# Kernel optimization log

Hardware: AMD Instinct MI355X
Metric: run time of the kernel (lower is better)

Reference implementation:

```python
import jax, jax.numpy as jnp
import numpy as np

E, M, B, S = 1024, 256, 4, 2048
LN_EPS = 1e-5

def _l2norm(x):
    # F.normalize(p=2, dim=-1, eps=1e-12)
    n = jnp.linalg.norm(x, axis=-1, keepdims=True)
    return x / jnp.maximum(n, 1e-12)

def _layernorm(x, g, b):
    mu = jnp.mean(x, axis=-1, keepdims=True)
    var = jnp.var(x, axis=-1, keepdims=True)
    return (x - mu) * jax.lax.rsqrt(var + LN_EPS) * g + b

def setup_inputs() -> dict:
    key = jax.random.key(0)
    ks = jax.random.split(key, 16)
    s = 0.02
    inp = {
        'x': jax.random.normal(ks[0], (B, S, E), jnp.float32),
        'memory': jnp.zeros((B, M, M), jnp.float32),
        'w_k': jax.random.normal(ks[1], (M, E), jnp.float32) * s,
        'b_k': jnp.zeros((M,), jnp.float32),
        'w_q': jax.random.normal(ks[2], (M, E), jnp.float32) * s,
        'b_q': jnp.zeros((M,), jnp.float32),
        'w_v': jax.random.normal(ks[3], (M, E), jnp.float32) * s,
        'b_v': jnp.zeros((M,), jnp.float32),
        'w_out': jax.random.normal(ks[4], (E, M), jnp.float32) * s,
        'b_out': jnp.zeros((E,), jnp.float32),
        'w_gw': jax.random.normal(ks[5], (1, E), jnp.float32) * s,
        'b_gw': jnp.full((1,), -2.0, jnp.float32),
        'w_gf': jax.random.normal(ks[6], (1, E), jnp.float32) * s,
        'b_gf': jnp.full((1,), 2.0, jnp.float32),
        'ln1_g': jnp.ones((E,), jnp.float32),
        'ln1_b': jnp.zeros((E,), jnp.float32),
        'ln2_g': jnp.ones((E,), jnp.float32),
        'ln2_b': jnp.zeros((E,), jnp.float32),
        'w_f1': jax.random.normal(ks[7], (4 * E, E), jnp.float32) * s,
        'b_f1': jnp.zeros((4 * E,), jnp.float32),
        'w_f2': jax.random.normal(ks[8], (E, 4 * E), jnp.float32) * s,
        'b_f2': jnp.zeros((E,), jnp.float32),
    }
    return inp

def reference(x, memory, w_k, b_k, w_q, b_q, w_v, b_v, w_out, b_out,
              w_gw, b_gw, w_gf, b_gf, ln1_g, ln1_b, ln2_g, ln2_b,
              w_f1, b_f1, w_f2, b_f2):
    xn = _layernorm(x, ln1_g, ln1_b)                      # [B,S,E]
    k_all = _l2norm(xn @ w_k.T + b_k)                     # [B,S,M]
    q_all = _l2norm(xn @ w_q.T + b_q)                     # [B,S,M]
    v_all = jnp.tanh(xn @ w_v.T + b_v)                    # [B,S,M]
    beta_all = jax.nn.sigmoid(xn @ w_gw.T + b_gw)         # [B,S,1]
    decay_all = jax.nn.sigmoid(xn @ w_gf.T + b_gf)        # [B,S,1]

    def step(mem, inps):
        k, q, v, beta, decay = inps                       # k,q,v:[B,M]; beta,decay:[B,1]
        readout = jnp.einsum('bij,bj->bi', mem, q)        # read BEFORE update
        assoc = v[:, :, None] * k[:, None, :]             # [B,M,M] outer product
        mem = decay[:, :, None] * mem + beta[:, :, None] * assoc
        return mem, readout

    seq = (jnp.swapaxes(k_all, 0, 1), jnp.swapaxes(q_all, 0, 1),
           jnp.swapaxes(v_all, 0, 1), jnp.swapaxes(beta_all, 0, 1),
           jnp.swapaxes(decay_all, 0, 1))
    new_memory, readouts = jax.lax.scan(step, memory, seq)  # readouts: [S,B,M]
    stacked = jnp.swapaxes(readouts, 0, 1)                  # [B,S,M]
    mixer_out = stacked @ w_out.T + b_out                   # [B,S,E]

    x = x + mixer_out
    h = _layernorm(x, ln2_g, ln2_b)
    ffn = jax.nn.gelu(h @ w_f1.T + b_f1, approximate=False) @ w_f2.T + b_f2
    x = x + ffn
    return (x, new_memory)
```

## Files before the change

### kernel.cpp

```cpp
#include <hip/hip_runtime.h>
#include <stdint.h>

#define E_DIM 1024
#define M_DIM 256
#define B_DIM 4
#define S_DIM 2048
#define NTOK  8192
#define CHUNK 64
#define NCHUNK 32
#define NCB   128

typedef unsigned short u16;
typedef unsigned int   u32;
typedef __attribute__((ext_vector_type(8))) short short8;
typedef __attribute__((ext_vector_type(4))) float floatx4;

#define OFF_WKQV   ((size_t)0)
#define OFF_WOUT   ((size_t)1572864)
#define OFF_WF1    ((size_t)2097152)
#define OFF_WF2    ((size_t)10485760)
#define OFF_BKQV   ((size_t)18874368)
#define OFF_BETA   ((size_t)18877440)
#define OFF_DECAY  ((size_t)18910208)
#define OFF_P      ((size_t)18942976)
#define OFF_WW     ((size_t)18976256)
#define OFF_ABUF   ((size_t)19009024)
#define OFF_XN     ((size_t)21106176)
#define OFF_KQV    ((size_t)37883392)
#define OFF_T      ((size_t)63049216)
#define OFF_STATES ((size_t)96603648)
#define OFF_RO     ((size_t)130158080)
#define OFF_H      OFF_XN
#define OFF_Y1     OFF_T
#define OFF_G      OFF_STATES

__device__ __forceinline__ u16 f2bf(float f) {
    union { float f; u32 u; } a; a.f = f;
    u32 u = a.u;
    return (u16)((u + 0x7fffu + ((u >> 16) & 1u)) >> 16);
}
__device__ __forceinline__ u32 pack2bf(float a, float b) {
    return (u32)f2bf(a) | ((u32)f2bf(b) << 16);
}
__device__ __forceinline__ float sigmoidf_(float x) { return 1.0f / (1.0f + expf(-x)); }

__device__ __forceinline__ void gload_lds16(const u16* g, u16* l) {
    __builtin_amdgcn_global_load_lds((const __attribute__((address_space(1))) void*)g,
                                     (__attribute__((address_space(3))) void*)l, 16, 0, 0);
}

__device__ __forceinline__ void block_reduce_2(float& a, float& b, float* red, int t) {
#pragma unroll
    for (int o = 32; o > 0; o >>= 1) { a += __shfl_xor(a, o); b += __shfl_xor(b, o); }
    if ((t & 63) == 0) { red[t >> 6] = a; red[4 + (t >> 6)] = b; }
    __syncthreads();
    a = red[0] + red[1] + red[2] + red[3];
    b = red[4] + red[5] + red[6] + red[7];
    __syncthreads();
}

__global__ void f2bf4_kernel(const float4* __restrict__ in, uint2* __restrict__ out, int n4) {
    int i = blockIdx.x * 256 + threadIdx.x;
    if (i < n4) {
        float4 v = in[i];
        uint2 o; o.x = pack2bf(v.x, v.y); o.y = pack2bf(v.z, v.w);
        out[i] = o;
    }
}
__global__ void pack_kqv_w(const float4* __restrict__ wk, const float4* __restrict__ wq,
                           const float4* __restrict__ wv, uint2* __restrict__ out) {
    int i = blockIdx.x * 256 + threadIdx.x;
    int sec = i >> 16;
    int off = i & 65535;
    const float4* src = (sec == 0) ? wk : ((sec == 1) ? wq : wv);
    float4 v = src[off];
    uint2 o; o.x = pack2bf(v.x, v.y); o.y = pack2bf(v.z, v.w);
    out[i] = o;
}
__global__ void pack_bias(const float* __restrict__ bk, const float* __restrict__ bq,
                          const float* __restrict__ bv, float* __restrict__ out) {
    int i = blockIdx.x * 256 + threadIdx.x;
    if (i < 256) out[i] = bk[i];
    else if (i < 512) out[i] = bq[i - 256];
    else out[i] = bv[i - 512];
}

__global__ __launch_bounds__(256) void ln1_gates(
    const float* __restrict__ x, const float* __restrict__ g, const float* __restrict__ b,
    const float* __restrict__ wgw, const float* __restrict__ bgw,
    const float* __restrict__ wgf, const float* __restrict__ bgf,
    u16* __restrict__ xn, float* __restrict__ beta, float* __restrict__ decay)
{
    __shared__ float red[8];
    const int row = blockIdx.x;
    const int t = threadIdx.x;
    const float4 v = ((const float4*)(x + (size_t)row * E_DIM))[t];
    float s  = v.x + v.y + v.z + v.w;
    float ss = v.x * v.x + v.y * v.y + v.z * v.z + v.w * v.w;
    block_reduce_2(s, ss, red, t);
    const float mean = s * (1.0f / E_DIM);
    const float var  = ss * (1.0f / E_DIM) - mean * mean;
    const float rstd = rsqrtf(var + 1e-5f);
    const float4 gg = ((const float4*)g)[t];
    const float4 bb = ((const float4*)b)[t];
    float4 xnv;
    xnv.x = (v.x - mean) * rstd * gg.x + bb.x;
    xnv.y = (v.y - mean) * rstd * gg.y + bb.y;
    xnv.z = (v.z - mean) * rstd * gg.z + bb.z;
    xnv.w = (v.w - mean) * rstd * gg.w + bb.w;
    uint2 o; o.x = pack2bf(xnv.x, xnv.y); o.y = pack2bf(xnv.z, xnv.w);
    ((uint2*)(xn + (size_t)row * E_DIM))[t] = o;
    const float4 w1 = ((const float4*)wgw)[t];
    const float4 w2 = ((const float4*)wgf)[t];
    float dg = xnv.x * w1.x + xnv.y * w1.y + xnv.z * w1.z + xnv.w * w1.w;
    float df = xnv.x * w2.x + xnv.y * w2.y + xnv.z * w2.z + xnv.w * w2.w;
    block_reduce_2(dg, df, red, t);
    if (t == 0) {
        beta[row]  = sigmoidf_(dg + bgw[0]);
        decay[row] = sigmoidf_(df + bgf[0]);
    }
}

__global__ __launch_bounds__(256) void ln2_kernel(
    const float* __restrict__ y1, const float* __restrict__ g, const float* __restrict__ b,
    u16* __restrict__ h)
{
    __shared__ float red[8];
    const int row = blockIdx.x;
    const int t = threadIdx.x;
    const float4 v = ((const float4*)(y1 + (size_t)row * E_DIM))[t];
    float s  = v.x + v.y + v.z + v.w;
    float ss = v.x * v.x + v.y * v.y + v.z * v.z + v.w * v.w;
    block_reduce_2(s, ss, red, t);
    const float mean = s * (1.0f / E_DIM);
    const float var  = ss * (1.0f / E_DIM) - mean * mean;
    const float rstd = rsqrtf(var + 1e-5f);
    const float4 gg = ((const float4*)g)[t];
    const float4 bb = ((const float4*)b)[t];
    float4 xnv;
    xnv.x = (v.x - mean) * rstd * gg.x + bb.x;
    xnv.y = (v.y - mean) * rstd * gg.y + bb.y;
    xnv.z = (v.z - mean) * rstd * gg.z + bb.z;
    xnv.w = (v.w - mean) * rstd * gg.w + bb.w;
    uint2 o; o.x = pack2bf(xnv.x, xnv.y); o.y = pack2bf(xnv.z, xnv.w);
    ((uint2*)(h + (size_t)row * E_DIM))[t] = o;
}

__global__ __launch_bounds__(256) void kqv_act(float* __restrict__ kqv) {
    __shared__ float red[8];
    const int row = blockIdx.x;
    const int t = threadIdx.x;
    float* p = kqv + (size_t)row * 768;
    float kv = p[t], qv = p[256 + t], vv = p[512 + t];
    float sk = kv * kv, sq = qv * qv;
    block_reduce_2(sk, sq, red, t);
    float nk = fmaxf(sqrtf(sk), 1e-12f);
    float nq = fmaxf(sqrtf(sq), 1e-12f);
    p[t]       = kv / nk;
    p[256 + t] = qv / nq;
    p[512 + t] = tanhf(vv);
}

__global__ void chunk_prep(const float* __restrict__ beta, const float* __restrict__ decay,
                           float* __restrict__ P, float* __restrict__ ww) {
    int cb = blockIdx.x;
    int b = cb >> 5, c = cb & 31;
    int tb = b * S_DIM + c * CHUNK;
    int j = threadIdx.x;
    __shared__ float d[64], bt[64], Ps[65];
    d[j]  = decay[tb + j];
    bt[j] = beta[tb + j];
    __syncthreads();
    if (j == 0) {
        float p = 1.0f; Ps[0] = 1.0f;
        for (int i = 0; i < 64; i++) { p *= d[i]; Ps[i + 1] = p; }
    }
    __syncthreads();
    P[cb * 65 + j] = Ps[j];
    if (j == 0) P[cb * 65 + 64] = Ps[64];
    ww[cb * 64 + j] = bt[j] / Ps[j + 1];
}

__global__ __launch_bounds__(256) void t_kernel(const float* __restrict__ kqv,
                                                const float* __restrict__ P,
                                                const float* __restrict__ ww,
                                                float* __restrict__ T) {
    int cb = blockIdx.y;
    int tile = blockIdx.x;
    int r0 = (tile >> 2) * 64, c0 = (tile & 3) * 64;
    int b = cb >> 5, c = cb & 31;
    int tb = b * S_DIM + c * CHUNK;
    float p64 = P[cb * 65 + 64];
    __shared__ float Vs[64][65], Ks[64][65];
    int t = threadIdx.x;
#pragma unroll
    for (int i = 0; i < 16; i++) {
        int idx = t + i * 256; int j = idx >> 6, col = idx & 63;
        float sc = ww[cb * 64 + j] * p64;
        Vs[j][col] = kqv[(size_t)(tb + j) * 768 + 512 + r0 + col] * sc;
        Ks[j][col] = kqv[(size_t)(tb + j) * 768 + 0   + c0 + col];
    }
    __syncthreads();
    int tr = t >> 4, tc = t & 15;
    float a[4][4] = {};
    for (int j = 0; j < 64; j++) {
        float vv[4], kk[4];
#pragma unroll
        for (int r = 0; r < 4; r++)  vv[r] = Vs[j][tr * 4 + r];
#pragma unroll
        for (int cc = 0; cc < 4; cc++) kk[cc] = Ks[j][tc * 4 + cc];
#pragma unroll
        for (int r = 0; r < 4; r++)
#pragma unroll
            for (int cc = 0; cc < 4; cc++) a[r][cc] += vv[r] * kk[cc];
    }
#pragma unroll
    for (int r = 0; r < 4; r++)
#pragma unroll
        for (int cc = 0; cc < 4; cc++)
            T[(size_t)cb * 65536 + (size_t)(r0 + tr * 4 + r) * 256 + (c0 + tc * 4 + cc)] = a[r][cc];
}

__global__ void mem_scan(const float* __restrict__ mem0, const float* __restrict__ T,
                         const float* __restrict__ P, float* __restrict__ states,
                         float* __restrict__ memOut) {
    int gid = blockIdx.x * 256 + threadIdx.x;
    int b = gid >> 16; int e = gid & 65535;
    float s = mem0[gid];
    for (int c = 0; c < NCHUNK; c++) {
        int cb = b * NCHUNK + c;
        states[(size_t)cb * 65536 + e] = s;
        s = P[cb * 65 + 64] * s + T[(size_t)cb * 65536 + e];
    }
    memOut[gid] = s;
}

__global__ __launch_bounds__(256) void qk_attn(const float* __restrict__ kqv,
                                               const float* __restrict__ P,
                                               const float* __restrict__ ww,
                                               float* __restrict__ Abuf) {
    int cb = blockIdx.x;
    int b = cb >> 5, c = cb & 31;
    int tb = b * S_DIM + c * CHUNK;
    __shared__ float Qs[64][65], Ks[64][65];
    int t = threadIdx.x;
    int tr = t >> 4, tc = t & 15;
    float acc[4][4] = {};
    for (int kt = 0; kt < 4; kt++) {
        __syncthreads();
#pragma unroll
        for (int i = 0; i < 16; i++) {
            int idx = t + i * 256; int rr = idx >> 6, cc2 = idx & 63;
            Qs[rr][cc2] = kqv[(size_t)(tb + rr) * 768 + 256 + kt * 64 + cc2];
            Ks[rr][cc2] = kqv[(size_t)(tb + rr) * 768 + 0   + kt * 64 + cc2];
        }
        __syncthreads();
        for (int kk = 0; kk < 64; kk++) {
            float qq[4], kx[4];
#pragma unroll
            for (int r = 0; r < 4; r++)  qq[r] = Qs[tr * 4 + r][kk];
#pragma unroll
            for (int cc = 0; cc < 4; cc++) kx[cc] = Ks[tc * 4 + cc][kk];
#pragma unroll
            for (int r = 0; r < 4; r++)
#pragma unroll
                for (int cc = 0; cc < 4; cc++) acc[r][cc] += qq[r] * kx[cc];
        }
    }
#pragma unroll
    for (int r = 0; r < 4; r++) {
#pragma unroll
        for (int cc = 0; cc < 4; cc++) {
            int i = tr * 4 + r, j = tc * 4 + cc;
            float v = (j < i) ? acc[r][cc] * (P[cb * 65 + i] * ww[cb * 64 + j]) : 0.0f;
            Abuf[(size_t)cb * 4096 + i * 64 + j] = v;
        }
    }
}

__global__ __launch_bounds__(256) void readout_k(const float* __restrict__ kqv,
                                                 const float* __restrict__ Abuf,
                                                 const float* __restrict__ states,
                                                 const float* __restrict__ P,
                                                 u16* __restrict__ ro) {
    int cb = blockIdx.y;
    int rt = blockIdx.x;
    int b = cb >> 5, c = cb & 31;
    int tb = b * S_DIM + c * CHUNK;
    int r0 = rt * 64;
    __shared__ float As[64][65], Vs[64][65], Qs[64][65], Ms[64][65];
    int t = threadIdx.x;
    int tr = t >> 4, tc = t & 15;
#pragma unroll
    for (int i = 0; i < 16; i++) {
        int idx = t + i * 256; int rr = idx >> 6, cc2 = idx & 63;
        As[rr][cc2] = Abuf[(size_t)cb * 4096 + rr * 64 + cc2];
        Vs[rr][cc2] = kqv[(size_t)(tb + rr) * 768 + 512 + r0 + cc2];
    }
    __syncthreads();
    float acc[4][4] = {};
    for (int j = 0; j < 64; j++) {
        float aa[4], vv[4];
#pragma unroll
        for (int r = 0; r < 4; r++)  aa[r] = As[tr * 4 + r][j];
#pragma unroll
        for (int cc = 0; cc < 4; cc++) vv[cc] = Vs[j][tc * 4 + cc];
#pragma unroll
        for (int r = 0; r < 4; r++)
#pragma unroll
            for (int cc = 0; cc < 4; cc++) acc[r][cc] += aa[r] * vv[cc];
    }
    float acc2[4][4] = {};
    for (int kt = 0; kt < 4; kt++) {
        __syncthreads();
#pragma unroll
        for (int i = 0; i < 16; i++) {
            int idx = t + i * 256; int rr = idx >> 6, cc2 = idx & 63;
            Qs[rr][cc2] = kqv[(size_t)(tb + rr) * 768 + 256 + kt * 64 + cc2];
            Ms[rr][cc2] = states[(size_t)cb * 65536 + (size_t)(r0 + rr) * 256 + kt * 64 + cc2];
        }
        __syncthreads();
        for (int kk = 0; kk < 64; kk++) {
            float qq[4], mm[4];
#pragma unroll
            for (int r = 0; r < 4; r++)  qq[r] = Qs[tr * 4 + r][kk];
#pragma unroll
            for (int cc = 0; cc < 4; cc++) mm[cc] = Ms[tc * 4 + cc][kk];
#pragma unroll
            for (int r = 0; r < 4; r++)
#pragma unroll
                for (int cc = 0; cc < 4; cc++) acc2[r][cc] += qq[r] * mm[cc];
        }
    }
#pragma unroll
    for (int r = 0; r < 4; r++) {
#pragma unroll
        for (int cc = 0; cc < 4; cc++) {
            int i = tr * 4 + r;
            float val = acc[r][cc] + P[cb * 65 + i] * acc2[r][cc];
            ro[(size_t)(tb + i) * 256 + r0 + tc * 4 + cc] = f2bf(val);
        }
    }
}

#define EPI_BIAS  0
#define EPI_RESID 1
#define EPI_GELU  2

template<int EPI>
__global__ __launch_bounds__(256) void gemm_bt(
    const u16* __restrict__ A, int lda,
    const u16* __restrict__ B, int ldb,
    const float* __restrict__ bias,
    const float* __restrict__ resid,
    float* __restrict__ outF, u16* __restrict__ outB,
    int ldc, int K)
{
    __shared__ u16 As[2][64 * 32];
    __shared__ u16 Bs[2][128 * 32];
    const int t = threadIdx.x;
    const int lane = t & 63;
    const int w = t >> 6;
    const int waveM = (w >> 1) * 32;
    const int waveN = (w & 1) * 64;
    const int m0 = blockIdx.y * 64;
    const int n0 = blockIdx.x * 128;

    const int sr = t >> 2, sc = (t & 3) * 8;
    const u16* Ag  = A + (size_t)(m0 + sr) * lda + sc;
    const u16* Bg0 = B + (size_t)(n0 + sr) * ldb + sc;
    const u16* Bg1 = B + (size_t)(n0 + 64 + sr) * ldb + sc;

    floatx4 acc[2][4] = {};

    const int kg = (lane >> 4) * 8;
    const int rsel = lane & 15;
    const int NK = K >> 5;

    gload_lds16(Ag, As[0] + t * 8);
    gload_lds16(Bg0, Bs[0] + t * 8);
    gload_lds16(Bg1, Bs[0] + (t + 256) * 8);

    for (int kt = 0; kt < NK; kt++) {
        __syncthreads();
        const int cur = kt & 1;
        if (kt + 1 < NK) {
            const int kof = (kt + 1) * 32;
            gload_lds16(Ag + kof, As[cur ^ 1] + t * 8);
            gload_lds16(Bg0 + kof, Bs[cur ^ 1] + t * 8);
            gload_lds16(Bg1 + kof, Bs[cur ^ 1] + (t + 256) * 8);
        }
        short8 af[2], bfr[4];
#pragma unroll
        for (int i = 0; i < 2; i++)
            af[i] = *(const short8*)(As[cur] + (waveM + i * 16 + rsel) * 32 + kg);
#pragma unroll
        for (int j = 0; j < 4; j++)
            bfr[j] = *(const short8*)(Bs[cur] + (waveN + j * 16 + rsel) * 32 + kg);
#pragma unroll
        for (int i = 0; i < 2; i++)
#pragma unroll
            for (int j = 0; j < 4; j++)
                acc[i][j] = __builtin_amdgcn_mfma_f32_16x16x32_bf16(af[i], bfr[j], acc[i][j], 0, 0, 0);
    }

    const int rbase = (lane >> 4) * 4;
#pragma unroll
    for (int i = 0; i < 2; i++) {
#pragma unroll
        for (int j = 0; j < 4; j++) {
            const int col = n0 + waveN + j * 16 + rsel;
            const float bv = bias[col];
#pragma unroll
            for (int r = 0; r < 4; r++) {
                const int row = m0 + waveM + i * 16 + rbase + r;
                const size_t oidx = (size_t)row * ldc + col;
                float v = acc[i][j][r] + bv;
                if (EPI == EPI_BIAS) {
                    outF[oidx] = v;
                } else if (EPI == EPI_RESID) {
                    outF[oidx] = v + resid[oidx];
                } else {
                    float gl = 0.5f * v * (1.0f + erff(v * 0.70710678118654752f));
                    outB[oidx] = f2bf(gl);
                }
            }
        }
    }
}

extern "C" void kernel_launch(void* const* d_in, const int* in_sizes, int n_in,
                              void* d_out, int out_size, void* d_ws, size_t ws_size,
                              hipStream_t stream) {
    const float* x     = (const float*)d_in[0];
    const float* mem0  = (const float*)d_in[1];
    const float* w_k   = (const float*)d_in[2];
    const float* b_k   = (const float*)d_in[3];
    const float* w_q   = (const float*)d_in[4];
    const float* b_q   = (const float*)d_in[5];
    const float* w_v   = (const float*)d_in[6];
    const float* b_v   = (const float*)d_in[7];
    const float* w_out = (const float*)d_in[8];
    const float* b_out = (const float*)d_in[9];
    const float* w_gw  = (const float*)d_in[10];
    const float* b_gw  = (const float*)d_in[11];
    const float* w_gf  = (const float*)d_in[12];
    const float* b_gf  = (const float*)d_in[13];
    const float* ln1g  = (const float*)d_in[14];
    const float* ln1b  = (const float*)d_in[15];
    const float* ln2g  = (const float*)d_in[16];
    const float* ln2b  = (const float*)d_in[17];
    const float* w_f1  = (const float*)d_in[18];
    const float* b_f1  = (const float*)d_in[19];
    const float* w_f2  = (const float*)d_in[20];
    const float* b_f2  = (const float*)d_in[21];

    char* ws = (char*)d_ws;
    u16*   wkqv  = (u16*)(ws + OFF_WKQV);
    u16*   wout  = (u16*)(ws + OFF_WOUT);
    u16*   wf1   = (u16*)(ws + OFF_WF1);
    u16*   wf2   = (u16*)(ws + OFF_WF2);
    float* bkqv  = (float*)(ws + OFF_BKQV);
    float* beta  = (float*)(ws + OFF_BETA);
    float* decay = (float*)(ws + OFF_DECAY);
    float* P     = (float*)(ws + OFF_P);
    float* ww    = (float*)(ws + OFF_WW);
    float* Abuf  = (float*)(ws + OFF_ABUF);
    u16*   xn    = (u16*)(ws + OFF_XN);
    float* kqv   = (float*)(ws + OFF_KQV);
    float* T     = (float*)(ws + OFF_T);
    float* states= (float*)(ws + OFF_STATES);
    u16*   ro    = (u16*)(ws + OFF_RO);
    u16*   h     = (u16*)(ws + OFF_H);
    float* y1    = (float*)(ws + OFF_Y1);
    u16*   g     = (u16*)(ws + OFF_G);

    float* out_x   = (float*)d_out;
    float* out_mem = out_x + (size_t)NTOK * E_DIM;

    pack_kqv_w<<<768, 256, 0, stream>>>((const float4*)w_k, (const float4*)w_q,
                                        (const float4*)w_v, (uint2*)wkqv);
    f2bf4_kernel<<<256, 256, 0, stream>>>((const float4*)w_out, (uint2*)wout, 1024 * 256 / 4);
    f2bf4_kernel<<<4096, 256, 0, stream>>>((const float4*)w_f1, (uint2*)wf1, 4096 * 1024 / 4);
    f2bf4_kernel<<<4096, 256, 0, stream>>>((const float4*)w_f2, (uint2*)wf2, 1024 * 4096 / 4);
    pack_bias<<<3, 256, 0, stream>>>(b_k, b_q, b_v, bkqv);

    ln1_gates<<<NTOK, 256, 0, stream>>>(x, ln1g, ln1b, w_gw, b_gw, w_gf, b_gf, xn, beta, decay);

    gemm_bt<EPI_BIAS><<<dim3(6, 128), 256, 0, stream>>>(xn, 1024, wkqv, 1024, bkqv, nullptr,
                                                        kqv, nullptr, 768, 1024);
    kqv_act<<<NTOK, 256, 0, stream>>>(kqv);

    chunk_prep<<<NCB, 64, 0, stream>>>(beta, decay, P, ww);
    t_kernel<<<dim3(16, NCB), 256, 0, stream>>>(kqv, P, ww, T);
    mem_scan<<<1024, 256, 0, stream>>>(mem0, T, P, states, out_mem);
    qk_attn<<<NCB, 256, 0, stream>>>(kqv, P, ww, Abuf);
    readout_k<<<dim3(4, NCB), 256, 0, stream>>>(kqv, Abuf, states, P, ro);

    gemm_bt<EPI_RESID><<<dim3(8, 128), 256, 0, stream>>>(ro, 256, wout, 256, b_out, x,
                                                         y1, nullptr, 1024, 256);
    ln2_kernel<<<NTOK, 256, 0, stream>>>(y1, ln2g, ln2b, h);
    gemm_bt<EPI_GELU><<<dim3(32, 128), 256, 0, stream>>>(h, 1024, wf1, 1024, b_f1, nullptr,
                                                         nullptr, g, 4096, 1024);
    gemm_bt<EPI_RESID><<<dim3(8, 128), 256, 0, stream>>>(g, 4096, wf2, 4096, b_f2, y1,
                                                         out_x, nullptr, 1024, 4096);
}
```

Measured before the change: 539.3 us.

## Swizzle GEMM LDS layout and use 128-row tiles for FFN1 GEMM

```diff
diff --git a/kernel.cpp b/kernel.cpp
--- a/kernel.cpp
+++ b/kernel.cpp
@@ -47,6 +47,13 @@
 __device__ __forceinline__ void gload_lds16(const u16* g, u16* l) {
     __builtin_amdgcn_global_load_lds((const __attribute__((address_space(1))) void*)g,
                                      (__attribute__((address_space(3))) void*)l, 16, 0, 0);
+}
+
+__device__ __forceinline__ int sw_slot(int idx) {
+    return ((idx & 3) ^ ((idx >> 3) & 3)) * 8;
+}
+__device__ __forceinline__ int sw_read(int row, int kc) {
+    return row * 32 + ((kc ^ ((row >> 1) & 3)) << 3);
 }
 
 __device__ __forceinline__ void block_reduce_2(float& a, float& b, float* red, int t) {
@@ -347,7 +354,7 @@
 #define EPI_RESID 1
 #define EPI_GELU  2
 
-template<int EPI>
+template<int EPI, int BM>
 __global__ __launch_bounds__(256) void gemm_bt(
     const u16* __restrict__ A, int lda,
     const u16* __restrict__ B, int ldb,
@@ -356,28 +363,31 @@
     float* __restrict__ outF, u16* __restrict__ outB,
     int ldc, int K)
 {
-    __shared__ u16 As[2][64 * 32];
+    constexpr int MI = BM / 32;
+    __shared__ u16 As[2][BM * 32];
     __shared__ u16 Bs[2][128 * 32];
     const int t = threadIdx.x;
     const int lane = t & 63;
     const int w = t >> 6;
-    const int waveM = (w >> 1) * 32;
+    const int waveM = (w >> 1) * (BM / 2);
     const int waveN = (w & 1) * 64;
-    const int m0 = blockIdx.y * 64;
+    const int m0 = blockIdx.y * BM;
     const int n0 = blockIdx.x * 128;
 
-    const int sr = t >> 2, sc = (t & 3) * 8;
-    const u16* Ag  = A + (size_t)(m0 + sr) * lda + sc;
-    const u16* Bg0 = B + (size_t)(n0 + sr) * ldb + sc;
-    const u16* Bg1 = B + (size_t)(n0 + 64 + sr) * ldb + sc;
-
-    floatx4 acc[2][4] = {};
-
-    const int kg = (lane >> 4) * 8;
+    const int sr = t >> 2, scw = sw_slot(t);
+    const u16* Ag0 = A + (size_t)(m0 + sr) * lda + scw;
+    const u16* Ag1 = A + (size_t)(m0 + 64 + sr) * lda + scw;
+    const u16* Bg0 = B + (size_t)(n0 + sr) * ldb + scw;
+    const u16* Bg1 = B + (size_t)(n0 + 64 + sr) * ldb + scw;
+
+    floatx4 acc[MI][4] = {};
+
+    const int kc = lane >> 4;
     const int rsel = lane & 15;
     const int NK = K >> 5;
 
-    gload_lds16(Ag, As[0] + t * 8);
+    gload_lds16(Ag0, As[0] + t * 8);
+    if (BM == 128) gload_lds16(Ag1, As[0] + (t + 256) * 8);
     gload_lds16(Bg0, Bs[0] + t * 8);
     gload_lds16(Bg1, Bs[0] + (t + 256) * 8);
 
@@ -386,19 +396,20 @@
         const int cur = kt & 1;
         if (kt + 1 < NK) {
             const int kof = (kt + 1) * 32;
-            gload_lds16(Ag + kof, As[cur ^ 1] + t * 8);
+            gload_lds16(Ag0 + kof, As[cur ^ 1] + t * 8);
+            if (BM == 128) gload_lds16(Ag1 + kof, As[cur ^ 1] + (t + 256) * 8);
             gload_lds16(Bg0 + kof, Bs[cur ^ 1] + t * 8);
             gload_lds16(Bg1 + kof, Bs[cur ^ 1] + (t + 256) * 8);
         }
-        short8 af[2], bfr[4];
-#pragma unroll
-        for (int i = 0; i < 2; i++)
-            af[i] = *(const short8*)(As[cur] + (waveM + i * 16 + rsel) * 32 + kg);
+        short8 af[MI], bfr[4];
+#pragma unroll
+        for (int i = 0; i < MI; i++)
+            af[i] = *(const short8*)(As[cur] + sw_read(waveM + i * 16 + rsel, kc));
 #pragma unroll
         for (int j = 0; j < 4; j++)
-            bfr[j] = *(const short8*)(Bs[cur] + (waveN + j * 16 + rsel) * 32 + kg);
-#pragma unroll
-        for (int i = 0; i < 2; i++)
+            bfr[j] = *(const short8*)(Bs[cur] + sw_read(waveN + j * 16 + rsel, kc));
+#pragma unroll
+        for (int i = 0; i < MI; i++)
 #pragma unroll
             for (int j = 0; j < 4; j++)
                 acc[i][j] = __builtin_amdgcn_mfma_f32_16x16x32_bf16(af[i], bfr[j], acc[i][j], 0, 0, 0);
@@ -406,7 +417,7 @@
 
     const int rbase = (lane >> 4) * 4;
 #pragma unroll
-    for (int i = 0; i < 2; i++) {
+    for (int i = 0; i < MI; i++) {
 #pragma unroll
         for (int j = 0; j < 4; j++) {
             const int col = n0 + waveN + j * 16 + rsel;
@@ -487,8 +498,8 @@
 
     ln1_gates<<<NTOK, 256, 0, stream>>>(x, ln1g, ln1b, w_gw, b_gw, w_gf, b_gf, xn, beta, decay);
 
-    gemm_bt<EPI_BIAS><<<dim3(6, 128), 256, 0, stream>>>(xn, 1024, wkqv, 1024, bkqv, nullptr,
-                                                        kqv, nullptr, 768, 1024);
+    gemm_bt<EPI_BIAS, 64><<<dim3(6, 128), 256, 0, stream>>>(xn, 1024, wkqv, 1024, bkqv, nullptr,
+                                                            kqv, nullptr, 768, 1024);
     kqv_act<<<NTOK, 256, 0, stream>>>(kqv);
 
     chunk_prep<<<NCB, 64, 0, stream>>>(beta, decay, P, ww);
@@ -497,11 +508,11 @@
     qk_attn<<<NCB, 256, 0, stream>>>(kqv, P, ww, Abuf);
     readout_k<<<dim3(4, NCB), 256, 0, stream>>>(kqv, Abuf, states, P, ro);
 
-    gemm_bt<EPI_RESID><<<dim3(8, 128), 256, 0, stream>>>(ro, 256, wout, 256, b_out, x,
-                                                         y1, nullptr, 1024, 256);
+    gemm_bt<EPI_RESID, 64><<<dim3(8, 128), 256, 0, stream>>>(ro, 256, wout, 256, b_out, x,
+                                                             y1, nullptr, 1024, 256);
     ln2_kernel<<<NTOK, 256, 0, stream>>>(y1, ln2g, ln2b, h);
-    gemm_bt<EPI_GELU><<<dim3(32, 128), 256, 0, stream>>>(h, 1024, wf1, 1024, b_f1, nullptr,
-                                                         nullptr, g, 4096, 1024);
-    gemm_bt<EPI_RESID><<<dim3(8, 128), 256, 0, stream>>>(g, 4096, wf2, 4096, b_f2, y1,
-                                                         out_x, nullptr, 1024, 4096);
-}
+    gemm_bt<EPI_GELU, 128><<<dim3(32, 64), 256, 0, stream>>>(h, 1024, wf1, 1024, b_f1, nullptr,
+                                                             nullptr, g, 4096, 1024);
+    gemm_bt<EPI_RESID, 64><<<dim3(8, 128), 256, 0, stream>>>(g, 4096, wf2, 4096, b_f2, y1,
+                                                             out_x, nullptr, 1024, 4096);
+}
```

Result: no change. 531.4 us (-1.5%).
